# Kernel tuning notes

Hardware: AMD Instinct MI355X
Metric: run time of the kernel (lower is better)

## Reference

```python
import jax, jax.numpy as jnp
import numpy as np

HID, FFN, E, K = 1024, 4096, 8, 2
CAP_FACTOR = 1.25


def setup_inputs() -> dict:
    key = jax.random.key(0)
    k1, k2, k3, k4 = jax.random.split(key, 4)
    B, T = 4, 2048
    x = jax.random.normal(k1, (B, T, HID), dtype=jnp.float32)
    router_w = jax.random.normal(k2, (E, HID), dtype=jnp.float32) * 0.02
    w1 = jax.random.normal(k3, (E, HID, FFN), dtype=jnp.float32) * 0.02
    w2 = jax.random.normal(k4, (E, FFN, HID), dtype=jnp.float32) * 0.02
    return {"x": x, "router_w": router_w, "w1": w1, "w2": w2}


def reference(x, router_w, w1, w2):
    B, T, H = x.shape
    N = B * T
    x_flat = x.reshape(N, H)
    # capacity per expert (static, shape-derived)
    C = max(1, int(CAP_FACTOR * N / E * K))

    # router (eval mode: no noise)
    logits = x_flat @ router_w.T                      # [N, E]
    probs = jax.nn.softmax(logits, axis=-1)
    top_v, top_i = jax.lax.top_k(probs, K)            # [N, K]
    top_v = top_v / jnp.sum(top_v, axis=-1, keepdims=True)

    out = jnp.zeros_like(x_flat)
    for k in range(K):
        eid = top_i[:, k]                             # [N] expert id per token
        gate = top_v[:, k]                            # [N]
        # position of each token within its expert, in token order
        onehot = jax.nn.one_hot(eid, E, dtype=jnp.int32)          # [N, E]
        pos = jnp.take_along_axis(jnp.cumsum(onehot, axis=0), eid[:, None], axis=1)[:, 0] - 1
        keep = pos < C                                # capacity drop (first C in token order)
        slot = jnp.where(keep, eid * C + pos, E * C)  # dropped tokens -> dump slot

        # dispatch: scatter kept tokens into per-expert capacity buffers
        buf = jnp.zeros((E * C + 1, H), dtype=x.dtype).at[slot].add(
            x_flat * keep[:, None].astype(x.dtype))
        expert_in = buf[: E * C].reshape(E, C, H)     # [E, C, H]

        # per-expert FFN (grouped GEMM -> GELU -> grouped GEMM)
        h = jax.nn.gelu(jnp.einsum('ech,ehf->ecf', expert_in, w1), approximate=False)
        y = jnp.einsum('ecf,efh->ech', h, w2)         # [E, C, H]

        # combine: gather back to token order, mask dropped, apply gate
        tok = y.reshape(E * C, H)[jnp.minimum(slot, E * C - 1)]
        out = out + tok * (gate * keep.astype(x.dtype))[:, None]

    return out.reshape(B, T, H)
```

## Files before the change

### kernel.cpp

```cpp
#include <hip/hip_runtime.h>
#include <hip/hip_bf16.h>
#include <math.h>

#define N_TOK 8192
#define HIDD  1024
#define FFND  4096
#define NE    8
#define CAP   2560
#define TMX   20
#define RMAX  16512

typedef __attribute__((ext_vector_type(4))) float  f32x4;
typedef __attribute__((ext_vector_type(8))) __bf16 bf16x8;

__device__ __forceinline__ unsigned short f2bf(float f) {
    unsigned u = __float_as_uint(f);
    u = (u + 0x7fffu + ((u >> 16) & 1u)) >> 16;
    return (unsigned short)u;
}

__device__ __forceinline__ void gld_lds16(const void* g, void* l) {
    __builtin_amdgcn_global_load_lds(
        (const __attribute__((address_space(1))) unsigned int*)g,
        (__attribute__((address_space(3))) unsigned int*)l, 16, 0, 0);
}

template <int R, int C>
__global__ __launch_bounds__(256) void transpose_cvt(const float* __restrict__ W,
                                                     unsigned short* __restrict__ Wt) {
    __shared__ unsigned short st[64][72];
    int e  = blockIdx.z;
    int r0 = blockIdx.y * 64, c0 = blockIdx.x * 64;
    int tid = threadIdx.x;
    int rb = tid >> 4, cq = tid & 15;
    const float* src = W + ((size_t)e * R + r0) * C + c0;
#pragma unroll
    for (int i = 0; i < 4; i++) {
        int kr = i * 16 + rb;
        float4 v = *reinterpret_cast<const float4*>(src + (size_t)kr * C + cq * 4);
        st[cq * 4 + 0][kr] = f2bf(v.x);
        st[cq * 4 + 1][kr] = f2bf(v.y);
        st[cq * 4 + 2][kr] = f2bf(v.z);
        st[cq * 4 + 3][kr] = f2bf(v.w);
    }
    __syncthreads();
    unsigned short* dst = Wt + ((size_t)e * C + c0) * R + r0;
#pragma unroll
    for (int i = 0; i < 4; i++) {
        int cr = i * 16 + rb;
        uint2 v = *reinterpret_cast<const uint2*>(&st[cr][cq * 4]);
        *reinterpret_cast<uint2*>(dst + (size_t)cr * R + cq * 4) = v;
    }
}

__global__ __launch_bounds__(256) void router_kernel(const float* __restrict__ x,
                                                     const float* __restrict__ rw,
                                                     unsigned short* __restrict__ xbf,
                                                     int* __restrict__ cnt,
                                                     int* __restrict__ tok,
                                                     float* __restrict__ gate) {
    __shared__ float4 rwl[2048];
    __shared__ int   e0s[32], e1s[32];
    __shared__ float g0s[32], g1s[32];
    __shared__ int   baseS[16];

    int tid = threadIdx.x, lane = tid & 63, w = tid >> 6;
    for (int i = tid; i < 2048; i += 256) rwl[i] = reinterpret_cast<const float4*>(rw)[i];
    __syncthreads();

    int tbase = blockIdx.x * 32 + w * 8;
    for (int i = 0; i < 8; i++) {
        int t = tbase + i;
        const float4* xr = reinterpret_cast<const float4*>(x) + (size_t)t * 256;
        float4 xv[4];
#pragma unroll
        for (int c = 0; c < 4; c++) xv[c] = xr[c * 64 + lane];
        uint2* xb = reinterpret_cast<uint2*>(xbf) + (size_t)t * 256;
#pragma unroll
        for (int c = 0; c < 4; c++) {
            uint2 p;
            p.x = (unsigned)f2bf(xv[c].x) | ((unsigned)f2bf(xv[c].y) << 16);
            p.y = (unsigned)f2bf(xv[c].z) | ((unsigned)f2bf(xv[c].w) << 16);
            xb[c * 64 + lane] = p;
        }
        float dot[NE];
#pragma unroll
        for (int e = 0; e < NE; e++) {
            float s = 0.f;
#pragma unroll
            for (int c = 0; c < 4; c++) {
                float4 a = rwl[e * 256 + c * 64 + lane];
                s += xv[c].x * a.x + xv[c].y * a.y + xv[c].z * a.z + xv[c].w * a.w;
            }
            dot[e] = s;
        }
#pragma unroll
        for (int e = 0; e < NE; e++) {
            float v = dot[e];
#pragma unroll
            for (int o = 32; o > 0; o >>= 1) v += __shfl_xor(v, o, 64);
            dot[e] = v;
        }
        if (lane == 0) {
            int e0 = 0; float l0 = dot[0];
#pragma unroll
            for (int e = 1; e < NE; e++) if (dot[e] > l0) { l0 = dot[e]; e0 = e; }
            int e1 = -1; float l1 = -3.4e38f;
#pragma unroll
            for (int e = 0; e < NE; e++) if (e != e0 && dot[e] > l1) { l1 = dot[e]; e1 = e; }
            float g0 = 1.f / (1.f + expf(l1 - l0));
            int j = w * 8 + i;
            e0s[j] = e0; e1s[j] = e1; g0s[j] = g0; g1s[j] = 1.f - g0;
        }
    }
    __syncthreads();

    int e0 = 255, e1 = 255, rank0 = 0, rank1 = 0, slotcnt = 0;
    float g0 = 0.f, g1 = 0.f;
    if (w == 0) {
        if (lane < 32) { e0 = e0s[lane]; e1 = e1s[lane]; g0 = g0s[lane]; g1 = g1s[lane]; }
        unsigned long long lt = (1ull << lane) - 1ull;
#pragma unroll
        for (int ee = 0; ee < NE; ee++) {
            unsigned long long m0 = __ballot(e0 == ee);
            unsigned long long m1 = __ballot(e1 == ee);
            if (e0 == ee) rank0 = (int)__popcll(m0 & lt);
            if (e1 == ee) rank1 = (int)__popcll(m1 & lt);
            if (lane == ee)      slotcnt = (int)__popcll(m0);
            if (lane == NE + ee) slotcnt = (int)__popcll(m1);
        }
        if (lane < 16) baseS[lane] = atomicAdd(&cnt[lane * 16], slotcnt);
    }
    __syncthreads();
    if (w == 0 && lane < 32) {
        int t = blockIdx.x * 32 + lane;
        int p0 = baseS[e0] + rank0;
        if (p0 < CAP) { tok[e0 * CAP + p0] = t; gate[e0 * CAP + p0] = g0; }
        int p1 = baseS[NE + e1] + rank1;
        if (p1 < CAP) { tok[(NE + e1) * CAP + p1] = t; gate[(NE + e1) * CAP + p1] = g1; }
    }
}

template <int KD, int ND, bool G1>
__global__ __launch_bounds__(256) void ffn_gemm_f(const unsigned short* __restrict__ A,
                                                  const unsigned short* __restrict__ Bw,
                                                  unsigned short* __restrict__ H,
                                                  float* __restrict__ O,
                                                  const int* __restrict__ cntAll,
                                                  const int* __restrict__ tokL,
                                                  const float* __restrict__ gateL,
                                                  int slot0, int pbase) {
    constexpr int TN = ND / 128;
    int bid = blockIdx.x;
    int tn  = bid % TN;
    int tme = bid / TN;
    int tm  = tme % TMX;
    int s   = slot0 + tme / TMX;
    int eW  = s & 7;
    int cnt_e = min(cntAll[s * 16], CAP);
    if (tm * 128 >= cnt_e) return;
    int off_e = 0;
#pragma unroll
    for (int i = 0; i < 16; i++) {
        int c = min(cntAll[i * 16], CAP);
        off_e += (i >= pbase && i < s) ? c : 0;
    }
    const int lbase = s * CAP;

    __shared__ __align__(16) unsigned short At[128 * 32];
    __shared__ __align__(16) unsigned short Bt[128 * 32];

    int tid = threadIdx.x;
    int w = tid >> 6, l = tid & 63;
    int wr = w >> 1, wc = w & 1;

    int r1 = tid >> 2, q1 = tid & 3;
    int r2 = r1 + 64;

    const char* aSrc1;
    const char* aSrc2;
    if (G1) {
        int p1 = tm * 128 + r1, p2 = tm * 128 + r2;
        int t1 = tokL[lbase + (p1 < cnt_e ? p1 : 0)];
        int t2 = tokL[lbase + (p2 < cnt_e ? p2 : 0)];
        aSrc1 = (const char*)(A + (size_t)t1 * KD) + ((q1 ^ ((r1 >> 1) & 3)) << 4);
        aSrc2 = (const char*)(A + (size_t)t2 * KD) + ((q1 ^ ((r2 >> 1) & 3)) << 4);
    } else {
        size_t row1 = (size_t)off_e + tm * 128 + r1;
        size_t row2 = row1 + 64;
        aSrc1 = (const char*)(A + row1 * KD) + ((q1 ^ ((r1 >> 1) & 3)) << 4);
        aSrc2 = (const char*)(A + row2 * KD) + ((q1 ^ ((r2 >> 1) & 3)) << 4);
    }
    const char* bSrc1 = (const char*)(Bw + ((size_t)eW * ND + tn * 128 + r1) * KD) + ((q1 ^ ((r1 >> 1) & 3)) << 4);
    const char* bSrc2 = (const char*)(Bw + ((size_t)eW * ND + tn * 128 + r2) * KD) + ((q1 ^ ((r2 >> 1) & 3)) << 4);

    char* aDst1 = (char*)At + w * 1024;
    char* aDst2 = aDst1 + 4096;
    char* bDst1 = (char*)Bt + w * 1024;
    char* bDst2 = bDst1 + 4096;

    int aro[4], bro[4];
#pragma unroll
    for (int m = 0; m < 4; m++) {
        int r = wr * 64 + m * 16 + (l & 15);
        aro[m] = r * 64 + (((l >> 4) ^ ((r >> 1) & 3)) << 4);
        int c = wc * 64 + m * 16 + (l & 15);
        bro[m] = c * 64 + (((l >> 4) ^ ((c >> 1) & 3)) << 4);
    }

    f32x4 zf = {0.f, 0.f, 0.f, 0.f};
    f32x4 acc[4][4];
#pragma unroll
    for (int m = 0; m < 4; m++)
#pragma unroll
        for (int n = 0; n < 4; n++) acc[m][n] = zf;

    for (int k0 = 0; k0 < KD; k0 += 32) {
        size_t kb = (size_t)k0 * 2;
        gld_lds16(aSrc1 + kb, aDst1);
        gld_lds16(aSrc2 + kb, aDst2);
        gld_lds16(bSrc1 + kb, bDst1);
        gld_lds16(bSrc2 + kb, bDst2);
        __syncthreads();
        bf16x8 af[4], bf[4];
#pragma unroll
        for (int m = 0; m < 4; m++) af[m] = *reinterpret_cast<const bf16x8*>((const char*)At + aro[m]);
#pragma unroll
        for (int n = 0; n < 4; n++) bf[n] = *reinterpret_cast<const bf16x8*>((const char*)Bt + bro[n]);
#pragma unroll
        for (int m = 0; m < 4; m++)
#pragma unroll
            for (int n = 0; n < 4; n++)
                acc[m][n] = __builtin_amdgcn_mfma_f32_16x16x32_bf16(af[m], bf[n], acc[m][n], 0, 0, 0);
        __syncthreads();
    }

    if (G1) {
#pragma unroll
        for (int m = 0; m < 4; m++) {
#pragma unroll
            for (int j = 0; j < 4; j++) {
                int rr = wr * 64 + m * 16 + (l >> 4) * 4 + j;
                int p = tm * 128 + rr;
                if (p < cnt_e) {
                    size_t row = (size_t)(off_e + p);
                    unsigned short* hp = H + row * ND + tn * 128 + wc * 64 + (l & 15);
#pragma unroll
                    for (int n = 0; n < 4; n++) {
                        float v = acc[m][n][j];
                        float g = 0.5f * v * (1.f + erff(v * 0.70710678118654752f));
                        hp[n * 16] = f2bf(g);
                    }
                }
            }
        }
    } else {
#pragma unroll
        for (int m = 0; m < 4; m++) {
#pragma unroll
            for (int j = 0; j < 4; j++) {
                int rr = wr * 64 + m * 16 + (l >> 4) * 4 + j;
                int p = tm * 128 + rr;
                if (p < cnt_e) {
                    int t = tokL[lbase + p];
                    float gv = gateL[lbase + p];
                    float* op = O + (size_t)t * ND + tn * 128 + wc * 64 + (l & 15);
#pragma unroll
                    for (int n = 0; n < 4; n++) atomicAdd(op + n * 16, gv * acc[m][n][j]);
                }
            }
        }
    }
}

template <int KD, int ND, bool G1>
__global__ __launch_bounds__(256) void ffn_gemm(const unsigned short* __restrict__ A,
                                                const float* __restrict__ W,
                                                unsigned short* __restrict__ H,
                                                float* __restrict__ O,
                                                const int* __restrict__ cntAll,
                                                const int* __restrict__ tokL,
                                                const float* __restrict__ gateL,
                                                int slot0, int pbase) {
    constexpr int TN = ND / 128;
    int bid = blockIdx.x;
    int tn  = bid % TN;
    int tme = bid / TN;
    int tm  = tme % TMX;
    int s   = slot0 + tme / TMX;
    int eW  = s & 7;
    int cnt_e = min(cntAll[s * 16], CAP);
    if (tm * 128 >= cnt_e) return;
    int off_e = 0;
#pragma unroll
    for (int i = 0; i < 16; i++) {
        int c = min(cntAll[i * 16], CAP);
        off_e += (i >= pbase && i < s) ? c : 0;
    }
    const int lbase = s * CAP;

    __shared__ __align__(16) unsigned short At[128 * 32];
    __shared__ __align__(16) unsigned short Bt[128 * 32];

    int tid = threadIdx.x;
    int w = tid >> 6, l = tid & 63;
    int wr = w >> 1, wc = w & 1;

    int r1 = tid >> 2, q1 = tid & 3;
    int r2 = r1 + 64;
    const char* aSrc1;
    const char* aSrc2;
    if (G1) {
        int p1 = tm * 128 + r1, p2 = tm * 128 + r2;
        int t1 = tokL[lbase + (p1 < cnt_e ? p1 : 0)];
        int t2 = tokL[lbase + (p2 < cnt_e ? p2 : 0)];
        aSrc1 = (const char*)(A + (size_t)t1 * KD) + ((q1 ^ ((r1 >> 1) & 3)) << 4);
        aSrc2 = (const char*)(A + (size_t)t2 * KD) + ((q1 ^ ((r2 >> 1) & 3)) << 4);
    } else {
        size_t row1 = (size_t)off_e + tm * 128 + r1;
        size_t row2 = row1 + 64;
        aSrc1 = (const char*)(A + row1 * KD) + ((q1 ^ ((r1 >> 1) & 3)) << 4);
        aSrc2 = (const char*)(A + row2 * KD) + ((q1 ^ ((r2 >> 1) & 3)) << 4);
    }
    char* aDst1 = (char*)At + w * 1024;
    char* aDst2 = aDst1 + 4096;

    const float* bSrc[4];
    int bOff[16];
#pragma unroll
    for (int j = 0; j < 4; j++) {
        int fidx = j * 1024 + tid * 4;
        int kk = fidx >> 7, n = fidx & 127;
        bSrc[j] = W + (size_t)eW * KD * ND + (size_t)kk * ND + tn * 128 + n;
#pragma unroll
        for (int i = 0; i < 4; i++) {
            int nn = n + i;
            bOff[j * 4 + i] = nn * 64 + ((((kk >> 3) ^ ((nn >> 1) & 3))) << 4) + ((kk & 7) << 1);
        }
    }

    int aro[4], bro[4];
#pragma unroll
    for (int m = 0; m < 4; m++) {
        int r = wr * 64 + m * 16 + (l & 15);
        aro[m] = r * 64 + (((l >> 4) ^ ((r >> 1) & 3)) << 4);
        int c = wc * 64 + m * 16 + (l & 15);
        bro[m] = c * 64 + (((l >> 4) ^ ((c >> 1) & 3)) << 4);
    }

    f32x4 zf = {0.f, 0.f, 0.f, 0.f};
    f32x4 acc[4][4];
#pragma unroll
    for (int m = 0; m < 4; m++)
#pragma unroll
        for (int n = 0; n < 4; n++) acc[m][n] = zf;

    for (int k0 = 0; k0 < KD; k0 += 32) {
        gld_lds16(aSrc1 + (size_t)k0 * 2, aDst1);
        gld_lds16(aSrc2 + (size_t)k0 * 2, aDst2);
        float4 bv[4];
#pragma unroll
        for (int j = 0; j < 4; j++) bv[j] = *reinterpret_cast<const float4*>(bSrc[j] + (size_t)k0 * ND);
        char* btc = (char*)Bt;
#pragma unroll
        for (int j = 0; j < 4; j++) {
            *(unsigned short*)(btc + bOff[j * 4 + 0]) = f2bf(bv[j].x);
            *(unsigned short*)(btc + bOff[j * 4 + 1]) = f2bf(bv[j].y);
            *(unsigned short*)(btc + bOff[j * 4 + 2]) = f2bf(bv[j].z);
            *(unsigned short*)(btc + bOff[j * 4 + 3]) = f2bf(bv[j].w);
        }
        __syncthreads();
        bf16x8 af[4], bf[4];
#pragma unroll
        for (int m = 0; m < 4; m++) af[m] = *reinterpret_cast<const bf16x8*>((const char*)At + aro[m]);
#pragma unroll
        for (int n = 0; n < 4; n++) bf[n] = *reinterpret_cast<const bf16x8*>((const char*)Bt + bro[n]);
#pragma unroll
        for (int m = 0; m < 4; m++)
#pragma unroll
            for (int n = 0; n < 4; n++)
                acc[m][n] = __builtin_amdgcn_mfma_f32_16x16x32_bf16(af[m], bf[n], acc[m][n], 0, 0, 0);
        __syncthreads();
    }

    if (G1) {
#pragma unroll
        for (int m = 0; m < 4; m++) {
#pragma unroll
            for (int j = 0; j < 4; j++) {
                int rr = wr * 64 + m * 16 + (l >> 4) * 4 + j;
                int p = tm * 128 + rr;
                if (p < cnt_e) {
                    size_t row = (size_t)(off_e + p);
                    unsigned short* hp = H + row * ND + tn * 128 + wc * 64 + (l & 15);
#pragma unroll
                    for (int n = 0; n < 4; n++) {
                        float v = acc[m][n][j];
                        float g = 0.5f * v * (1.f + erff(v * 0.70710678118654752f));
                        hp[n * 16] = f2bf(g);
                    }
                }
            }
        }
    } else {
#pragma unroll
        for (int m = 0; m < 4; m++) {
#pragma unroll
            for (int j = 0; j < 4; j++) {
                int rr = wr * 64 + m * 16 + (l >> 4) * 4 + j;
                int p = tm * 128 + rr;
                if (p < cnt_e) {
                    int t = tokL[lbase + p];
                    float gv = gateL[lbase + p];
                    float* op = O + (size_t)t * ND + tn * 128 + wc * 64 + (l & 15);
#pragma unroll
                    for (int n = 0; n < 4; n++) atomicAdd(op + n * 16, gv * acc[m][n][j]);
                }
            }
        }
    }
}

extern "C" void kernel_launch(void* const* d_in, const int* in_sizes, int n_in,
                              void* d_out, int out_size, void* d_ws, size_t ws_size,
                              hipStream_t stream) {
    const float* x  = (const float*)d_in[0];
    const float* rw = (const float*)d_in[1];
    const float* w1 = (const float*)d_in[2];
    const float* w2 = (const float*)d_in[3];
    float* out = (float*)d_out;
    char* ws = (char*)d_ws;

    int*   cnt  = (int*)ws;
    int*   tok  = (int*)(ws + 4096);
    float* gate = (float*)(ws + 4096 + 16 * CAP * 4);
    unsigned short* xbf = (unsigned short*)(ws + (1 << 20));
    size_t hOff = (1 << 20) + (size_t)N_TOK * HIDD * 2;
    unsigned short* h = (unsigned short*)(ws + hOff);

    size_t w1tSz = (size_t)NE * HIDD * FFND * 2;
    size_t hBig = (size_t)RMAX * FFND * 2;
    size_t hMid = (size_t)8448 * FFND * 2;
    size_t needBig = hOff + hBig + 2 * w1tSz;
    size_t needMid = hOff + hMid + 2 * w1tSz;

    hipMemsetAsync(cnt, 0, 1024, stream);
    hipMemsetAsync(d_out, 0, (size_t)N_TOK * HIDD * 4, stream);

    hipLaunchKernelGGL(router_kernel, dim3(N_TOK / 32), dim3(256), 0, stream,
                       x, rw, xbf, cnt, tok, gate);

    if (ws_size >= needMid) {
        size_t hSz = (ws_size >= needBig) ? hBig : hMid;
        unsigned short* w1t = (unsigned short*)(ws + hOff + hSz);
        unsigned short* w2t = (unsigned short*)(ws + hOff + hSz + w1tSz);
        hipLaunchKernelGGL((transpose_cvt<HIDD, FFND>), dim3(FFND / 64, HIDD / 64, NE), dim3(256), 0, stream, w1, w1t);
        hipLaunchKernelGGL((transpose_cvt<FFND, HIDD>), dim3(HIDD / 64, FFND / 64, NE), dim3(256), 0, stream, w2, w2t);
        if (ws_size >= needBig) {
            hipLaunchKernelGGL((ffn_gemm_f<HIDD, FFND, true>), dim3(16 * TMX * (FFND / 128)), dim3(256), 0, stream,
                               xbf, w1t, h, (float*)nullptr, cnt, tok, gate, 0, 0);
            hipLaunchKernelGGL((ffn_gemm_f<FFND, HIDD, false>), dim3(16 * TMX * (HIDD / 128)), dim3(256), 0, stream,
                               h, w2t, (unsigned short*)nullptr, out, cnt, tok, gate, 0, 0);
        } else {
            for (int k = 0; k < 2; k++) {
                hipLaunchKernelGGL((ffn_gemm_f<HIDD, FFND, true>), dim3(8 * TMX * (FFND / 128)), dim3(256), 0, stream,
                                   xbf, w1t, h, (float*)nullptr, cnt, tok, gate, 8 * k, 8 * k);
                hipLaunchKernelGGL((ffn_gemm_f<FFND, HIDD, false>), dim3(8 * TMX * (HIDD / 128)), dim3(256), 0, stream,
                                   h, w2t, (unsigned short*)nullptr, out, cnt, tok, gate, 8 * k, 8 * k);
            }
        }
    } else {
        for (int k = 0; k < 2; k++) {
            hipLaunchKernelGGL((ffn_gemm<HIDD, FFND, true>), dim3(8 * TMX * (FFND / 128)), dim3(256), 0, stream,
                               xbf, w1, h, (float*)nullptr, cnt, tok, gate, 8 * k, 8 * k);
            hipLaunchKernelGGL((ffn_gemm<FFND, HIDD, false>), dim3(8 * TMX * (HIDD / 128)), dim3(256), 0, stream,
                               h, w2, (unsigned short*)nullptr, out, cnt, tok, gate, 8 * k, 8 * k);
        }
    }
}
```

Measured before the change: 592.2 us.

## Remap grouped GEMM blocks so both k-slots of an expert are co-scheduled

Changes the block-index mapping in the bf16 grouped GEMM so consecutive blocks cycle over experts and each expert's two top-k slots share a chunk of CH column tiles. Blocks that reuse the same expert weights and token rows are launched close together, which should improve L2 reuse of weights and activations and leave fewer idle early-exit blocks in the middle of the grid. The mid-size workspace path is removed, so a smaller workspace now falls back to the slower fp32-weight kernel.

Result: faster. 558.8 us (-5.6%).

```diff
diff --git a/kernel.cpp b/kernel.cpp
--- a/kernel.cpp
+++ b/kernel.cpp
@@ -141,30 +141,36 @@
     }
 }
 
-template <int KD, int ND, bool G1>
+template <int KD, int ND, bool G1, int CH>
 __global__ __launch_bounds__(256) void ffn_gemm_f(const unsigned short* __restrict__ A,
                                                   const unsigned short* __restrict__ Bw,
                                                   unsigned short* __restrict__ H,
                                                   float* __restrict__ O,
                                                   const int* __restrict__ cntAll,
                                                   const int* __restrict__ tokL,
-                                                  const float* __restrict__ gateL,
-                                                  int slot0, int pbase) {
+                                                  const float* __restrict__ gateL) {
     constexpr int TN = ND / 128;
-    int bid = blockIdx.x;
-    int tn  = bid % TN;
-    int tme = bid / TN;
-    int tm  = tme % TMX;
-    int s   = slot0 + tme / TMX;
-    int eW  = s & 7;
-    int cnt_e = min(cntAll[s * 16], CAP);
-    if (tm * 128 >= cnt_e) return;
+    int e = blockIdx.x & 7;
+    int i = blockIdx.x >> 3;
+    int cnt0 = min(cntAll[e * 16], CAP);
+    int cnt1 = min(cntAll[(e + 8) * 16], CAP);
+    int tmx0 = (cnt0 + 127) >> 7;
+    int tmx1 = (cnt1 + 127) >> 7;
+    int tmsum = tmx0 + tmx1;
+    if (tmsum == 0) return;
+    int per_chunk = tmsum * CH;
+    int c = i / per_chunk;
+    if (c >= TN / CH) return;
+    int r = i - c * per_chunk;
+    int s, tm, cnt_e;
+    int t0 = tmx0 * CH;
+    if (r < t0) { s = e;     tm = r / CH; r -= tm * CH; cnt_e = cnt0; }
+    else { r -= t0; s = e + 8; tm = r / CH; r -= tm * CH; cnt_e = cnt1; }
+    int tn = c * CH + r;
+
     int off_e = 0;
 #pragma unroll
-    for (int i = 0; i < 16; i++) {
-        int c = min(cntAll[i * 16], CAP);
-        off_e += (i >= pbase && i < s) ? c : 0;
-    }
+    for (int t = 0; t < 16; t++) off_e += (t < s) ? min(cntAll[t * 16], CAP) : 0;
     const int lbase = s * CAP;
 
     __shared__ __align__(16) unsigned short At[128 * 32];
@@ -191,8 +197,8 @@
         aSrc1 = (const char*)(A + row1 * KD) + ((q1 ^ ((r1 >> 1) & 3)) << 4);
         aSrc2 = (const char*)(A + row2 * KD) + ((q1 ^ ((r2 >> 1) & 3)) << 4);
     }
-    const char* bSrc1 = (const char*)(Bw + ((size_t)eW * ND + tn * 128 + r1) * KD) + ((q1 ^ ((r1 >> 1) & 3)) << 4);
-    const char* bSrc2 = (const char*)(Bw + ((size_t)eW * ND + tn * 128 + r2) * KD) + ((q1 ^ ((r2 >> 1) & 3)) << 4);
+    const char* bSrc1 = (const char*)(Bw + ((size_t)e * ND + tn * 128 + r1) * KD) + ((q1 ^ ((r1 >> 1) & 3)) << 4);
+    const char* bSrc2 = (const char*)(Bw + ((size_t)e * ND + tn * 128 + r2) * KD) + ((q1 ^ ((r2 >> 1) & 3)) << 4);
 
     char* aDst1 = (char*)At + w * 1024;
     char* aDst2 = aDst1 + 4096;
@@ -202,10 +208,10 @@
     int aro[4], bro[4];
 #pragma unroll
     for (int m = 0; m < 4; m++) {
-        int r = wr * 64 + m * 16 + (l & 15);
-        aro[m] = r * 64 + (((l >> 4) ^ ((r >> 1) & 3)) << 4);
-        int c = wc * 64 + m * 16 + (l & 15);
-        bro[m] = c * 64 + (((l >> 4) ^ ((c >> 1) & 3)) << 4);
+        int rr = wr * 64 + m * 16 + (l & 15);
+        aro[m] = rr * 64 + (((l >> 4) ^ ((rr >> 1) & 3)) << 4);
+        int cc = wc * 64 + m * 16 + (l & 15);
+        bro[m] = cc * 64 + (((l >> 4) ^ ((cc >> 1) & 3)) << 4);
     }
 
     f32x4 zf = {0.f, 0.f, 0.f, 0.f};
@@ -342,10 +348,10 @@
     int aro[4], bro[4];
 #pragma unroll
     for (int m = 0; m < 4; m++) {
-        int r = wr * 64 + m * 16 + (l & 15);
-        aro[m] = r * 64 + (((l >> 4) ^ ((r >> 1) & 3)) << 4);
-        int c = wc * 64 + m * 16 + (l & 15);
-        bro[m] = c * 64 + (((l >> 4) ^ ((c >> 1) & 3)) << 4);
+        int rr = wr * 64 + m * 16 + (l & 15);
+        aro[m] = rr * 64 + (((l >> 4) ^ ((rr >> 1) & 3)) << 4);
+        int cc = wc * 64 + m * 16 + (l & 15);
+        bro[m] = cc * 64 + (((l >> 4) ^ ((cc >> 1) & 3)) << 4);
     }
 
     f32x4 zf = {0.f, 0.f, 0.f, 0.f};
@@ -440,9 +446,7 @@
 
     size_t w1tSz = (size_t)NE * HIDD * FFND * 2;
     size_t hBig = (size_t)RMAX * FFND * 2;
-    size_t hMid = (size_t)8448 * FFND * 2;
     size_t needBig = hOff + hBig + 2 * w1tSz;
-    size_t needMid = hOff + hMid + 2 * w1tSz;
 
     hipMemsetAsync(cnt, 0, 1024, stream);
     hipMemsetAsync(d_out, 0, (size_t)N_TOK * HIDD * 4, stream);
@@ -450,25 +454,15 @@
     hipLaunchKernelGGL(router_kernel, dim3(N_TOK / 32), dim3(256), 0, stream,
                        x, rw, xbf, cnt, tok, gate);
 
-    if (ws_size >= needMid) {
-        size_t hSz = (ws_size >= needBig) ? hBig : hMid;
-        unsigned short* w1t = (unsigned short*)(ws + hOff + hSz);
-        unsigned short* w2t = (unsigned short*)(ws + hOff + hSz + w1tSz);
+    if (ws_size >= needBig) {
+        unsigned short* w1t = (unsigned short*)(ws + hOff + hBig);
+        unsigned short* w2t = (unsigned short*)(ws + hOff + hBig + w1tSz);
         hipLaunchKernelGGL((transpose_cvt<HIDD, FFND>), dim3(FFND / 64, HIDD / 64, NE), dim3(256), 0, stream, w1, w1t);
         hipLaunchKernelGGL((transpose_cvt<FFND, HIDD>), dim3(HIDD / 64, FFND / 64, NE), dim3(256), 0, stream, w2, w2t);
-        if (ws_size >= needBig) {
-            hipLaunchKernelGGL((ffn_gemm_f<HIDD, FFND, true>), dim3(16 * TMX * (FFND / 128)), dim3(256), 0, stream,
-                               xbf, w1t, h, (float*)nullptr, cnt, tok, gate, 0, 0);
-            hipLaunchKernelGGL((ffn_gemm_f<FFND, HIDD, false>), dim3(16 * TMX * (HIDD / 128)), dim3(256), 0, stream,
-                               h, w2t, (unsigned short*)nullptr, out, cnt, tok, gate, 0, 0);
-        } else {
-            for (int k = 0; k < 2; k++) {
-                hipLaunchKernelGGL((ffn_gemm_f<HIDD, FFND, true>), dim3(8 * TMX * (FFND / 128)), dim3(256), 0, stream,
-                                   xbf, w1t, h, (float*)nullptr, cnt, tok, gate, 8 * k, 8 * k);
-                hipLaunchKernelGGL((ffn_gemm_f<FFND, HIDD, false>), dim3(8 * TMX * (HIDD / 128)), dim3(256), 0, stream,
-                                   h, w2t, (unsigned short*)nullptr, out, cnt, tok, gate, 8 * k, 8 * k);
-            }
-        }
+        hipLaunchKernelGGL((ffn_gemm_f<HIDD, FFND, true, 8>), dim3(8 * 2 * TMX * (FFND / 128)), dim3(256), 0, stream,
+                           xbf, w1t, h, (float*)nullptr, cnt, tok, gate);
+        hipLaunchKernelGGL((ffn_gemm_f<FFND, HIDD, false, 4>), dim3(8 * 2 * TMX * (HIDD / 128)), dim3(256), 0, stream,
+                           h, w2t, (unsigned short*)nullptr, out, cnt, tok, gate);
     } else {
         for (int k = 0; k < 2; k++) {
             hipLaunchKernelGGL((ffn_gemm<HIDD, FFND, true>), dim3(8 * TMX * (FFND / 128)), dim3(256), 0, stream,
```
